# Performance work log

Hardware: AMD Instinct MI355X
Metric: run time of the kernel (lower is better)

The kernel has to match this reference:

```python
import jax, jax.numpy as jnp
import numpy as np

B, L, K, I, O = 4, 10000, 16, 256, 256


def setup_inputs() -> dict:
    key = jax.random.key(0)
    k1, k2, k3 = jax.random.split(key, 3)
    x = jax.random.normal(k1, (B, L, I), dtype=jnp.float32)
    index_tensor = jax.random.randint(k2, (L, K), 0, L, dtype=jnp.int64)
    stdv = 0.5
    mask = jax.random.uniform(k3, (K, I, O), dtype=jnp.float32, minval=-stdv, maxval=stdv)
    bias = jnp.zeros((O,), dtype=jnp.float32)
    return {"x": x, "index_tensor": index_tensor, "mask": mask, "bias": bias}


def reference(x, index_tensor, mask, bias):
    # torch: expand x to [b,l,l,i], gather along dim2 with index[l,k] -> [b,l,k,i]
    # equivalent: per output node n, neighbors x[:, index_tensor[n, j], :]
    gathered = x[:, index_tensor, :]            # [b, l, k, i]
    # flatten(k,i) @ flatten(mask: [k*i, o]) == einsum over k,i
    y = jnp.einsum('blki,kio->blo', gathered, mask) + bias
    return y
```

## Files before the change

kernel.cpp:

```cpp
#include <hip/hip_runtime.h>

#define Bdim 4
#define Ldim 10000
#define Kdim 16
#define Idim 256
#define Odim 256

typedef __attribute__((ext_vector_type(8))) __bf16 bf16x8;
typedef __attribute__((ext_vector_type(4))) float f32x4;

__global__ __launch_bounds__(256)
void prepack(const float* __restrict__ x, const float* __restrict__ mask,
             __bf16* __restrict__ xb, __bf16* __restrict__ wpk)
{
    const int b = blockIdx.x;
    if (b < 2500) {
        const size_t base = ((size_t)b * 256 + threadIdx.x) * 16;
#pragma unroll
        for (int j = 0; j < 2; ++j) {
            const float4 f0 = *(const float4*)(x + base + j * 8);
            const float4 f1 = *(const float4*)(x + base + j * 8 + 4);
            bf16x8 v;
            v[0] = (__bf16)f0.x; v[1] = (__bf16)f0.y; v[2] = (__bf16)f0.z; v[3] = (__bf16)f0.w;
            v[4] = (__bf16)f1.x; v[5] = (__bf16)f1.y; v[6] = (__bf16)f1.z; v[7] = (__bf16)f1.w;
            *(bf16x8*)(xb + base + j * 8) = v;
        }
    } else {
        const int tg = (b - 2500) * 256 + threadIdx.x;
        const int c  = tg >> 6;
        const int ln = tg & 63;
        const int ni  = c & 3;
        const int ks  = (c >> 2) & 1;
        const int wid = (c >> 3) & 3;
        const int kb  = c >> 5;
        const int n   = wid * 64 + ni * 16 + (ln & 15);
        const int kk0 = kb * 64 + ks * 32 + (ln >> 4) * 8;
        bf16x8 v;
#pragma unroll
        for (int j = 0; j < 8; ++j)
            v[j] = (__bf16)mask[(size_t)(kk0 + j) * Odim + n];
        *(bf16x8*)(wpk + (size_t)tg * 8) = v;
    }
}

#define TL 16
#define BM 64
#define LDA 72

__global__ __launch_bounds__(256, 3)
void piconv_gemm(const __bf16* __restrict__ xb,
                 const int* __restrict__ idxT,
                 const __bf16* __restrict__ wpk,
                 const float* __restrict__ bias,
                 float* __restrict__ out)
{
    __shared__ __bf16 Alds[2][BM * LDA];
    __shared__ int    idx_lds[TL * Kdim];

    const int t    = threadIdx.x;
    const int l0   = blockIdx.x * TL;
    const int lane = t & 63;
    const int wid  = t >> 6;
    const int q    = lane >> 4;
    const int r16  = lane & 15;

    idx_lds[t] = idxT[l0 * Kdim + t];

    const int arow  = t >> 2;
    const int apart = t & 3;
    const int alt   = arow & 15;
    const int abb   = arow >> 4;
    const size_t abase = ((size_t)abb * Ldim) << 8;

    const __bf16* wbase = wpk + ((size_t)(wid * 8) << 9) + lane * 8;

    f32x4  acc[4][4] = {};
    bf16x8 aN0, aN1, wA[8], wB[8];

    __syncthreads();

    {
        const int iv = idx_lds[alt * Kdim];
        const __bf16* s = xb + abase + (((size_t)iv) << 8) + apart * 16;
        aN0 = *(const bf16x8*)s;
        aN1 = *(const bf16x8*)(s + 8);
#pragma unroll
        for (int j = 0; j < 8; ++j)
            wA[j] = *(const bf16x8*)(wbase + j * 512);
    }

#define STEP(KB, BUF, WCUR, WNXT, PF)                                           \
    {                                                                           \
        *(bf16x8*)&Alds[BUF][arow * LDA + apart * 16]     = aN0;                \
        *(bf16x8*)&Alds[BUF][arow * LDA + apart * 16 + 8] = aN1;                \
        __syncthreads();                                                        \
        if (PF) {                                                               \
            const int kn = ((KB) + 1) >> 2;                                     \
            const int io = ((((KB) + 1) & 3) << 6) + apart * 16;                \
            const int iv = idx_lds[alt * Kdim + kn];                            \
            const __bf16* s = xb + abase + (((size_t)iv) << 8) + io;            \
            aN0 = *(const bf16x8*)s;                                            \
            aN1 = *(const bf16x8*)(s + 8);                                      \
            const __bf16* wq = wbase + ((size_t)((KB) + 1)) * 16384;            \
            _Pragma("unroll")                                                   \
            for (int j = 0; j < 8; ++j)                                         \
                WNXT[j] = *(const bf16x8*)(wq + j * 512);                       \
        }                                                                       \
        _Pragma("unroll")                                                       \
        for (int ks = 0; ks < 2; ++ks) {                                        \
            bf16x8 af[4];                                                       \
            _Pragma("unroll")                                                   \
            for (int mi = 0; mi < 4; ++mi)                                      \
                af[mi] = *(bf16x8*)&Alds[BUF][(mi * 16 + r16) * LDA + ks * 32 + q * 8]; \
            _Pragma("unroll")                                                   \
            for (int mi = 0; mi < 4; ++mi)                                      \
                _Pragma("unroll")                                               \
                for (int ni = 0; ni < 4; ++ni)                                  \
                    acc[mi][ni] = __builtin_amdgcn_mfma_f32_16x16x32_bf16(      \
                        af[mi], WCUR[ks * 4 + ni], acc[mi][ni], 0, 0, 0);       \
        }                                                                       \
    }

    for (int kb2 = 0; kb2 < 32; ++kb2) {
        STEP(2 * kb2,     0, wA, wB, true)
        STEP(2 * kb2 + 1, 1, wB, wA, (2 * kb2 + 1) < 63)
    }
#undef STEP

    float bv[4];
#pragma unroll
    for (int ni = 0; ni < 4; ++ni)
        bv[ni] = bias[wid * 64 + ni * 16 + r16];
#pragma unroll
    for (int mi = 0; mi < 4; ++mi) {
#pragma unroll
        for (int rr = 0; rr < 4; ++rr) {
            const int lt = q * 4 + rr;
            float* dst = out + (((size_t)(mi * Ldim + l0 + lt)) << 8) + wid * 64 + r16;
#pragma unroll
            for (int ni = 0; ni < 4; ++ni)
                dst[ni * 16] = acc[mi][ni][rr] + bv[ni];
        }
    }
}

#define FTL 32
#define FBN 128
#define FLDA 72
__global__ __launch_bounds__(256)
void piconv_fallback(const float* __restrict__ x,
                     const int* __restrict__ idxT,
                     const float* __restrict__ mask,
                     const float* __restrict__ bias,
                     float* __restrict__ out)
{
    __shared__ __bf16 Alds[128 * FLDA];
    __shared__ __bf16 Wlds[FBN * FLDA];
    const int t  = threadIdx.x;
    const int l0 = blockIdx.x * FTL;
    const int n0 = blockIdx.y * FBN;
    const int lane = t & 63;
    const int wid  = t >> 6;
    const int wm   = wid >> 1;
    const int wn   = wid & 1;
    const int q    = lane >> 4;
    const int r16  = lane & 15;
    f32x4 acc[4][4] = {};
    const int am    = t >> 1;
    const int ahalf = t & 1;
    const int alt   = am & 31;
    const int abb   = am >> 5;
    const int al    = l0 + alt;
    const bool avalid = (al < Ldim);
    for (int kb = 0; kb < 64; ++kb) {
        {
            const int ksl = kb >> 2;
            const int i0  = ((kb & 3) << 6) + (ahalf << 5);
            const int idx = avalid ? idxT[al * Kdim + ksl] : 0;
            const float* src = x + (((size_t)(abb * Ldim + idx)) << 8) + i0;
#pragma unroll
            for (int j = 0; j < 4; ++j) {
                const float4 f0 = *(const float4*)(src + j * 8);
                const float4 f1 = *(const float4*)(src + j * 8 + 4);
                bf16x8 v;
                v[0] = (__bf16)f0.x; v[1] = (__bf16)f0.y; v[2] = (__bf16)f0.z; v[3] = (__bf16)f0.w;
                v[4] = (__bf16)f1.x; v[5] = (__bf16)f1.y; v[6] = (__bf16)f1.z; v[7] = (__bf16)f1.w;
                *(bf16x8*)&Alds[am * FLDA + (ahalf << 5) + j * 8] = v;
            }
        }
        {
#pragma unroll
            for (int it = 0; it < 4; ++it) {
                const int pair = t + it * 256;
                const int n    = pair & 127;
                const int g    = pair >> 7;
                const float* src = mask + (((size_t)(kb * 64 + g * 8)) << 8) + n0 + n;
                bf16x8 v;
#pragma unroll
                for (int j = 0; j < 8; ++j)
                    v[j] = (__bf16)src[(size_t)j << 8];
                *(bf16x8*)&Wlds[n * FLDA + g * 8] = v;
            }
        }
        __syncthreads();
#pragma unroll
        for (int ks = 0; ks < 2; ++ks) {
            bf16x8 af[4], bfr[4];
#pragma unroll
            for (int mi = 0; mi < 4; ++mi)
                af[mi] = *(bf16x8*)&Alds[(wm * 64 + mi * 16 + r16) * FLDA + ks * 32 + q * 8];
#pragma unroll
            for (int ni = 0; ni < 4; ++ni)
                bfr[ni] = *(bf16x8*)&Wlds[(wn * 64 + ni * 16 + r16) * FLDA + ks * 32 + q * 8];
#pragma unroll
            for (int mi = 0; mi < 4; ++mi)
#pragma unroll
                for (int ni = 0; ni < 4; ++ni)
                    acc[mi][ni] = __builtin_amdgcn_mfma_f32_16x16x32_bf16(
                        af[mi], bfr[ni], acc[mi][ni], 0, 0, 0);
        }
        __syncthreads();
    }
    float bv[4];
#pragma unroll
    for (int ni = 0; ni < 4; ++ni)
        bv[ni] = bias[n0 + wn * 64 + ni * 16 + r16];
#pragma unroll
    for (int mi = 0; mi < 4; ++mi) {
        const int mrow = wm * 64 + mi * 16 + q * 4;
#pragma unroll
        for (int rr = 0; rr < 4; ++rr) {
            const int m  = mrow + rr;
            const int lt = m & 31;
            const int bb = m >> 5;
            const int l  = l0 + lt;
            if (l < Ldim) {
                float* dst = out + (((size_t)(bb * Ldim + l)) << 8) + n0 + wn * 64 + r16;
#pragma unroll
                for (int ni = 0; ni < 4; ++ni)
                    dst[ni * 16] = acc[mi][ni][rr] + bv[ni];
            }
        }
    }
}

extern "C" void kernel_launch(void* const* d_in, const int* in_sizes, int n_in,
                              void* d_out, int out_size, void* d_ws, size_t ws_size,
                              hipStream_t stream) {
    const float* x    = (const float*)d_in[0];
    const int*   idx  = (const int*)d_in[1];
    const float* mask = (const float*)d_in[2];
    const float* bias = (const float*)d_in[3];
    float* out = (float*)d_out;

    const size_t xb_bytes = (size_t)Bdim * Ldim * Idim * 2;
    const size_t wp_bytes = (size_t)Kdim * Idim * Odim * 2;

    if (ws_size >= xb_bytes + wp_bytes) {
        __bf16* xb  = (__bf16*)d_ws;
        __bf16* wpk = (__bf16*)((char*)d_ws + xb_bytes);
        prepack<<<2500 + 512, 256, 0, stream>>>(x, mask, xb, wpk);
        piconv_gemm<<<Ldim / TL, 256, 0, stream>>>(xb, idx, wpk, bias, out);
    } else {
        dim3 grid((Ldim + FTL - 1) / FTL, Odim / FBN, 1);
        piconv_fallback<<<grid, 256, 0, stream>>>(x, idx, mask, bias, out);
    }
}
```

Before: 191.6 us.

## Deepen gathered-A prefetch to two steps and use lighter LDS barrier

```diff
diff --git a/kernel.cpp b/kernel.cpp
--- a/kernel.cpp
+++ b/kernel.cpp
@@ -47,6 +47,9 @@
 #define BM 64
 #define LDA 72
 
+#define BARRIER() do { asm volatile("s_waitcnt lgkmcnt(0)" ::: "memory"); \
+                       __builtin_amdgcn_s_barrier(); } while (0)
+
 __global__ __launch_bounds__(256, 3)
 void piconv_gemm(const __bf16* __restrict__ xb,
                  const int* __restrict__ idxT,
@@ -75,32 +78,39 @@
     const __bf16* wbase = wpk + ((size_t)(wid * 8) << 9) + lane * 8;
 
     f32x4  acc[4][4] = {};
-    bf16x8 aN0, aN1, wA[8], wB[8];
+    bf16x8 a0lo, a0hi;
+    bf16x8 a1lo, a1hi;
+    bf16x8 wA[8], wB[8];
 
     __syncthreads();
 
     {
         const int iv = idx_lds[alt * Kdim];
-        const __bf16* s = xb + abase + (((size_t)iv) << 8) + apart * 16;
-        aN0 = *(const bf16x8*)s;
-        aN1 = *(const bf16x8*)(s + 8);
+        const __bf16* s0 = xb + abase + (((size_t)iv) << 8) + apart * 16;
+        a0lo = *(const bf16x8*)s0;
+        a0hi = *(const bf16x8*)(s0 + 8);
 #pragma unroll
         for (int j = 0; j < 8; ++j)
             wA[j] = *(const bf16x8*)(wbase + j * 512);
-    }
-
-#define STEP(KB, BUF, WCUR, WNXT, PF)                                           \
+        const __bf16* s1 = s0 + 64;
+        a1lo = *(const bf16x8*)s1;
+        a1hi = *(const bf16x8*)(s1 + 8);
+    }
+
+#define STEP(KB, BUF, ALO, AHI, WCUR, WNXT, PFA, PFW)                           \
     {                                                                           \
-        *(bf16x8*)&Alds[BUF][arow * LDA + apart * 16]     = aN0;                \
-        *(bf16x8*)&Alds[BUF][arow * LDA + apart * 16 + 8] = aN1;                \
-        __syncthreads();                                                        \
-        if (PF) {                                                               \
-            const int kn = ((KB) + 1) >> 2;                                     \
-            const int io = ((((KB) + 1) & 3) << 6) + apart * 16;                \
+        *(bf16x8*)&Alds[BUF][arow * LDA + apart * 16]     = ALO;                \
+        *(bf16x8*)&Alds[BUF][arow * LDA + apart * 16 + 8] = AHI;                \
+        BARRIER();                                                              \
+        if (PFA) {                       \
+            const int kn = ((KB) + 2) >> 2;                                     \
+            const int io = ((((KB) + 2) & 3) << 6) + apart * 16;                \
             const int iv = idx_lds[alt * Kdim + kn];                            \
             const __bf16* s = xb + abase + (((size_t)iv) << 8) + io;            \
-            aN0 = *(const bf16x8*)s;                                            \
-            aN1 = *(const bf16x8*)(s + 8);                                      \
+            ALO = *(const bf16x8*)s;                                            \
+            AHI = *(const bf16x8*)(s + 8);                                      \
+        }                                                                       \
+        if (PFW) {                                                 \
             const __bf16* wq = wbase + ((size_t)((KB) + 1)) * 16384;            \
             _Pragma("unroll")                                                   \
             for (int j = 0; j < 8; ++j)                                         \
@@ -121,10 +131,12 @@
         }                                                                       \
     }
 
-    for (int kb2 = 0; kb2 < 32; ++kb2) {
-        STEP(2 * kb2,     0, wA, wB, true)
-        STEP(2 * kb2 + 1, 1, wB, wA, (2 * kb2 + 1) < 63)
-    }
+    for (int kb2 = 0; kb2 < 31; ++kb2) {
+        STEP(2 * kb2,     0, a0lo, a0hi, wA, wB, true, true)
+        STEP(2 * kb2 + 1, 1, a1lo, a1hi, wB, wA, true, true)
+    }
+    STEP(62, 0, a0lo, a0hi, wA, wB, false, true)
+    STEP(63, 1, a1lo, a1hi, wB, wA, false, false)
 #undef STEP
 
     float bv[4];
```

Measured after the change: 184.9 us. 1.04x faster.

## Halve GEMM row tile, deepen A prefetch to two stages, use lighter barrier

Applied to the files above, without the earlier changes.

```diff
diff --git a/kernel.cpp b/kernel.cpp
--- a/kernel.cpp
+++ b/kernel.cpp
@@ -43,11 +43,14 @@
     }
 }
 
-#define TL 16
-#define BM 64
+#define TL 8
+#define BM 32
 #define LDA 72
 
-__global__ __launch_bounds__(256, 3)
+#define BARRIER() do { asm volatile("s_waitcnt lgkmcnt(0)" ::: "memory"); \
+                       __builtin_amdgcn_s_barrier(); } while (0)
+
+__global__ __launch_bounds__(256, 4)
 void piconv_gemm(const __bf16* __restrict__ xb,
                  const int* __restrict__ idxT,
                  const __bf16* __restrict__ wpk,
@@ -64,56 +67,57 @@
     const int q    = lane >> 4;
     const int r16  = lane & 15;
 
-    idx_lds[t] = idxT[l0 * Kdim + t];
-
-    const int arow  = t >> 2;
-    const int apart = t & 3;
-    const int alt   = arow & 15;
-    const int abb   = arow >> 4;
+    if (t < TL * Kdim)
+        idx_lds[t] = idxT[l0 * Kdim + t];
+
+    const int arow = t >> 3;
+    const int apart = t & 7;
+    const int alt  = arow & 7;
+    const int abb  = arow >> 3;
     const size_t abase = ((size_t)abb * Ldim) << 8;
 
     const __bf16* wbase = wpk + ((size_t)(wid * 8) << 9) + lane * 8;
 
-    f32x4  acc[4][4] = {};
-    bf16x8 aN0, aN1, wA[8], wB[8];
+    f32x4  acc[2][4] = {};
+    bf16x8 a0, a1;
+    bf16x8 wA[8], wB[8];
 
     __syncthreads();
 
     {
         const int iv = idx_lds[alt * Kdim];
-        const __bf16* s = xb + abase + (((size_t)iv) << 8) + apart * 16;
-        aN0 = *(const bf16x8*)s;
-        aN1 = *(const bf16x8*)(s + 8);
+        const __bf16* s0 = xb + abase + (((size_t)iv) << 8) + apart * 8;
+        a0 = *(const bf16x8*)s0;
 #pragma unroll
         for (int j = 0; j < 8; ++j)
             wA[j] = *(const bf16x8*)(wbase + j * 512);
-    }
-
-#define STEP(KB, BUF, WCUR, WNXT, PF)                                           \
+        a1 = *(const bf16x8*)(s0 + 64);
+    }
+
+#define STEP(S, BUF, AV, WCUR, WNXT, PFA, PFW)                                  \
     {                                                                           \
-        *(bf16x8*)&Alds[BUF][arow * LDA + apart * 16]     = aN0;                \
-        *(bf16x8*)&Alds[BUF][arow * LDA + apart * 16 + 8] = aN1;                \
-        __syncthreads();                                                        \
-        if (PF) {                                                               \
-            const int kn = ((KB) + 1) >> 2;                                     \
-            const int io = ((((KB) + 1) & 3) << 6) + apart * 16;                \
+        *(bf16x8*)&Alds[BUF][arow * LDA + apart * 8] = AV;                      \
+        BARRIER();                                                              \
+        if (PFA) {                        \
+            const int kn = ((S) + 2) >> 2;                                      \
+            const int io = ((((S) + 2) & 3) << 6) + apart * 8;                  \
             const int iv = idx_lds[alt * Kdim + kn];                            \
-            const __bf16* s = xb + abase + (((size_t)iv) << 8) + io;            \
-            aN0 = *(const bf16x8*)s;                                            \
-            aN1 = *(const bf16x8*)(s + 8);                                      \
-            const __bf16* wq = wbase + ((size_t)((KB) + 1)) * 16384;            \
+            AV = *(const bf16x8*)(xb + abase + (((size_t)iv) << 8) + io);       \
+        }                                                                       \
+        if (PFW) {                                                  \
+            const __bf16* wq = wbase + ((size_t)((S) + 1)) * 16384;             \
             _Pragma("unroll")                                                   \
             for (int j = 0; j < 8; ++j)                                         \
                 WNXT[j] = *(const bf16x8*)(wq + j * 512);                       \
         }                                                                       \
         _Pragma("unroll")                                                       \
         for (int ks = 0; ks < 2; ++ks) {                                        \
-            bf16x8 af[4];                                                       \
+            bf16x8 af[2];                                                       \
             _Pragma("unroll")                                                   \
-            for (int mi = 0; mi < 4; ++mi)                                      \
+            for (int mi = 0; mi < 2; ++mi)                                      \
                 af[mi] = *(bf16x8*)&Alds[BUF][(mi * 16 + r16) * LDA + ks * 32 + q * 8]; \
             _Pragma("unroll")                                                   \
-            for (int mi = 0; mi < 4; ++mi)                                      \
+            for (int mi = 0; mi < 2; ++mi)                                      \
                 _Pragma("unroll")                                               \
                 for (int ni = 0; ni < 4; ++ni)                                  \
                     acc[mi][ni] = __builtin_amdgcn_mfma_f32_16x16x32_bf16(      \
@@ -121,10 +125,12 @@
         }                                                                       \
     }
 
-    for (int kb2 = 0; kb2 < 32; ++kb2) {
-        STEP(2 * kb2,     0, wA, wB, true)
-        STEP(2 * kb2 + 1, 1, wB, wA, (2 * kb2 + 1) < 63)
-    }
+    for (int s2 = 0; s2 < 31; ++s2) {
+        STEP(2 * s2,     0, a0, wA, wB, true, true)
+        STEP(2 * s2 + 1, 1, a1, wB, wA, true, true)
+    }
+    STEP(62, 0, a0, wA, wB, false, true)
+    STEP(63, 1, a1, wB, wA, false, false)
 #undef STEP
 
     float bv[4];
@@ -132,11 +138,13 @@
     for (int ni = 0; ni < 4; ++ni)
         bv[ni] = bias[wid * 64 + ni * 16 + r16];
 #pragma unroll
-    for (int mi = 0; mi < 4; ++mi) {
+    for (int mi = 0; mi < 2; ++mi) {
 #pragma unroll
         for (int rr = 0; rr < 4; ++rr) {
-            const int lt = q * 4 + rr;
-            float* dst = out + (((size_t)(mi * Ldim + l0 + lt)) << 8) + wid * 64 + r16;
+            const int g  = mi * 16 + q * 4 + rr;
+            const int bb = g >> 3;
+            const int lt = g & 7;
+            float* dst = out + (((size_t)(bb * Ldim + l0 + lt)) << 8) + wid * 64 + r16;
 #pragma unroll
             for (int ni = 0; ni < 4; ++ni)
                 dst[ni * 16] = acc[mi][ni][rr] + bv[ni];
```

Measured after the change: 211.2 us. 10.2% more time.

## Load gathered A fragments directly to registers and split output columns across grid

Applied to the files above, without the earlier changes.

```diff
diff --git a/kernel.cpp b/kernel.cpp
--- a/kernel.cpp
+++ b/kernel.cpp
@@ -44,101 +44,106 @@
 }
 
 #define TL 16
-#define BM 64
-#define LDA 72
-
-__global__ __launch_bounds__(256, 3)
+#define IDXS 17
+
+__global__ __launch_bounds__(128, 3)
 void piconv_gemm(const __bf16* __restrict__ xb,
                  const int* __restrict__ idxT,
                  const __bf16* __restrict__ wpk,
                  const float* __restrict__ bias,
                  float* __restrict__ out)
 {
-    __shared__ __bf16 Alds[2][BM * LDA];
-    __shared__ int    idx_lds[TL * Kdim];
+    __shared__ int idx_lds[TL * IDXS];
 
     const int t    = threadIdx.x;
     const int l0   = blockIdx.x * TL;
+    const int nh   = blockIdx.y;
     const int lane = t & 63;
-    const int wid  = t >> 6;
+    const int w    = t >> 6;
     const int q    = lane >> 4;
     const int r16  = lane & 15;
-
-    idx_lds[t] = idxT[l0 * Kdim + t];
-
-    const int arow  = t >> 2;
-    const int apart = t & 3;
-    const int alt   = arow & 15;
-    const int abb   = arow >> 4;
-    const size_t abase = ((size_t)abb * Ldim) << 8;
-
-    const __bf16* wbase = wpk + ((size_t)(wid * 8) << 9) + lane * 8;
-
-    f32x4  acc[4][4] = {};
-    bf16x8 aN0, aN1, wA[8], wB[8];
+    const int qo   = q * 8;
+
+#pragma unroll
+    for (int it = 0; it < 2; ++it) {
+        const int e = t + it * 128;
+        idx_lds[(e >> 4) * IDXS + (e & 15)] = idxT[l0 * Kdim + e];
+    }
+
+    const size_t abase0 = (size_t)(w * 2 + 0) * Ldim * Idim;
+    const size_t abase1 = (size_t)(w * 2 + 1) * Ldim * Idim;
+    const __bf16* wb = wpk + (size_t)nh * 8192 + lane * 8;
+
+    f32x4  acc[2][8] = {};
+    bf16x8 aE[2], aO[2];
+    bf16x8 wA[8], wB[8];
 
     __syncthreads();
 
     {
-        const int iv = idx_lds[alt * Kdim];
-        const __bf16* s = xb + abase + (((size_t)iv) << 8) + apart * 16;
-        aN0 = *(const bf16x8*)s;
-        aN1 = *(const bf16x8*)(s + 8);
-#pragma unroll
-        for (int j = 0; j < 8; ++j)
-            wA[j] = *(const bf16x8*)(wbase + j * 512);
-    }
-
-#define STEP(KB, BUF, WCUR, WNXT, PF)                                           \
+        const int iv = idx_lds[r16 * IDXS];
+        const __bf16* s = xb + abase0 + (((size_t)iv) << 8) + qo;
+        aE[0] = *(const bf16x8*)(s);
+        aO[0] = *(const bf16x8*)(s + 32);
+        const __bf16* s1 = xb + abase1 + (((size_t)iv) << 8) + qo;
+        aE[1] = *(const bf16x8*)(s1);
+        aO[1] = *(const bf16x8*)(s1 + 32);
+#pragma unroll
+        for (int j = 0; j < 4; ++j) {
+            wA[j]     = *(const bf16x8*)(wb + j * 512);
+            wA[j + 4] = *(const bf16x8*)(wb + 4096 + j * 512);
+        }
+    }
+
+#define STEPZ(S, ACUR, WCUR, WNXT, PFA, PFW)                                    \
     {                                                                           \
-        *(bf16x8*)&Alds[BUF][arow * LDA + apart * 16]     = aN0;                \
-        *(bf16x8*)&Alds[BUF][arow * LDA + apart * 16 + 8] = aN1;                \
-        __syncthreads();                                                        \
-        if (PF) {                                                               \
-            const int kn = ((KB) + 1) >> 2;                                     \
-            const int io = ((((KB) + 1) & 3) << 6) + apart * 16;                \
-            const int iv = idx_lds[alt * Kdim + kn];                            \
-            const __bf16* s = xb + abase + (((size_t)iv) << 8) + io;            \
-            aN0 = *(const bf16x8*)s;                                            \
-            aN1 = *(const bf16x8*)(s + 8);                                      \
-            const __bf16* wq = wbase + ((size_t)((KB) + 1)) * 16384;            \
+        int iv_pf = 0;                                                          \
+        if (PFA) iv_pf = idx_lds[r16 * IDXS + (((S) + 2) >> 3)];                \
+        if (PFW) {                                                              \
+            const __bf16* wq = wb + (size_t)(((S) + 1) >> 1) * 16384            \
+                                  + (((S) + 1) & 1) * 2048;                     \
             _Pragma("unroll")                                                   \
-            for (int j = 0; j < 8; ++j)                                         \
-                WNXT[j] = *(const bf16x8*)(wq + j * 512);                       \
+            for (int j = 0; j < 4; ++j) {                                       \
+                WNXT[j]     = *(const bf16x8*)(wq + j * 512);                   \
+                WNXT[j + 4] = *(const bf16x8*)(wq + 4096 + j * 512);            \
+            }                                                                   \
         }                                                                       \
         _Pragma("unroll")                                                       \
-        for (int ks = 0; ks < 2; ++ks) {                                        \
-            bf16x8 af[4];                                                       \
+        for (int mi = 0; mi < 2; ++mi)                                          \
             _Pragma("unroll")                                                   \
-            for (int mi = 0; mi < 4; ++mi)                                      \
-                af[mi] = *(bf16x8*)&Alds[BUF][(mi * 16 + r16) * LDA + ks * 32 + q * 8]; \
-            _Pragma("unroll")                                                   \
-            for (int mi = 0; mi < 4; ++mi)                                      \
-                _Pragma("unroll")                                               \
-                for (int ni = 0; ni < 4; ++ni)                                  \
-                    acc[mi][ni] = __builtin_amdgcn_mfma_f32_16x16x32_bf16(      \
-                        af[mi], WCUR[ks * 4 + ni], acc[mi][ni], 0, 0, 0);       \
+            for (int ni = 0; ni < 8; ++ni)                                      \
+                acc[mi][ni] = __builtin_amdgcn_mfma_f32_16x16x32_bf16(          \
+                    ACUR[mi], WCUR[ni], acc[mi][ni], 0, 0, 0);                  \
+        if (PFA) {                                                              \
+            const int io = (((S) + 2) & 7) * 32 + qo;                           \
+            ACUR[0] = *(const bf16x8*)(xb + abase0 + (((size_t)iv_pf) << 8) + io); \
+            ACUR[1] = *(const bf16x8*)(xb + abase1 + (((size_t)iv_pf) << 8) + io); \
         }                                                                       \
     }
 
-    for (int kb2 = 0; kb2 < 32; ++kb2) {
-        STEP(2 * kb2,     0, wA, wB, true)
-        STEP(2 * kb2 + 1, 1, wB, wA, (2 * kb2 + 1) < 63)
-    }
-#undef STEP
-
-    float bv[4];
-#pragma unroll
-    for (int ni = 0; ni < 4; ++ni)
-        bv[ni] = bias[wid * 64 + ni * 16 + r16];
-#pragma unroll
-    for (int mi = 0; mi < 4; ++mi) {
+    for (int s2 = 0; s2 < 63; ++s2) {
+        const int S = 2 * s2;
+        STEPZ(S,     aE, wA, wB, true, true)
+        STEPZ(S + 1, aO, wB, wA, true, true)
+        __builtin_amdgcn_s_barrier();
+    }
+    STEPZ(126, aE, wA, wB, false, true)
+    STEPZ(127, aO, wB, wA, false, false)
+#undef STEPZ
+
+    float bv[8];
+#pragma unroll
+    for (int ni = 0; ni < 8; ++ni)
+        bv[ni] = bias[nh * 128 + ni * 16 + r16];
+#pragma unroll
+    for (int mi = 0; mi < 2; ++mi) {
 #pragma unroll
         for (int rr = 0; rr < 4; ++rr) {
             const int lt = q * 4 + rr;
-            float* dst = out + (((size_t)(mi * Ldim + l0 + lt)) << 8) + wid * 64 + r16;
-#pragma unroll
-            for (int ni = 0; ni < 4; ++ni)
+            float* dst = out + (((size_t)((w * 2 + mi) * Ldim + l0 + lt)) << 8)
+                             + nh * 128 + r16;
+#pragma unroll
+            for (int ni = 0; ni < 8; ++ni)
                 dst[ni * 16] = acc[mi][ni][rr] + bv[ni];
         }
     }
@@ -260,7 +265,8 @@
         __bf16* xb  = (__bf16*)d_ws;
         __bf16* wpk = (__bf16*)((char*)d_ws + xb_bytes);
         prepack<<<2500 + 512, 256, 0, stream>>>(x, mask, xb, wpk);
-        piconv_gemm<<<Ldim / TL, 256, 0, stream>>>(xb, idx, wpk, bias, out);
+        dim3 ggrid(Ldim / TL, 2, 1);
+        piconv_gemm<<<ggrid, 128, 0, stream>>>(xb, idx, wpk, bias, out);
     } else {
         dim3 grid((Ldim + FTL - 1) / FTL, Odim / FBN, 1);
         piconv_fallback<<<grid, 256, 0, stream>>>(x, idx, mask, bias, out);
```

New measurement: 258.6 us. +35.0%, slower.
